# Performance work log

Hardware: AMD Instinct MI355X
Metric: run time of the kernel (lower is better)

The kernel has to match this reference:

```python
import jax, jax.numpy as jnp
import numpy as np

# Config mirrors init_kwargs
D_IN, D_OUT, HEADS, SEQ, BATCH = 1024, 64, 16, 2048, 2


def setup_inputs() -> dict:
    key = jax.random.key(0)
    kx, kq, kk, kv = jax.random.split(key, 4)
    scale = 1.0 / np.sqrt(D_IN)
    x = jax.random.normal(kx, (BATCH, SEQ, D_IN), dtype=jnp.float32)
    # Stacked per-head projection weights, [H, d_in, d_out] (qkv_bias=False)
    Wq = jax.random.normal(kq, (HEADS, D_IN, D_OUT), dtype=jnp.float32) * scale
    Wk = jax.random.normal(kk, (HEADS, D_IN, D_OUT), dtype=jnp.float32) * scale
    Wv = jax.random.normal(kv, (HEADS, D_IN, D_OUT), dtype=jnp.float32) * scale
    return {"x": x, "Wq": Wq, "Wk": Wk, "Wv": Wv}


def reference(x, Wq, Wk, Wv):
    # x: [B, S, d_in]; W*: [H, d_in, d_out]
    q = jnp.einsum("bsd,hde->bhse", x, Wq)
    k = jnp.einsum("bsd,hde->bhse", x, Wk)
    v = jnp.einsum("bsd,hde->bhse", x, Wv)
    scores = jnp.einsum("bhse,bhte->bhst", q, k) / jnp.sqrt(
        jnp.asarray(D_OUT, dtype=q.dtype)
    )
    S = x.shape[1]
    causal = jnp.tril(jnp.ones((S, S), dtype=bool))  # [S, S]
    scores = jnp.where(causal[None, None], scores, -jnp.inf)
    attn = jax.nn.softmax(scores, axis=-1)  # dropout=0.0 (eval)
    ctx = jnp.einsum("bhst,bhte->bhse", attn, v)  # [B, H, S, d_out]
    # concat heads on last dim -> [B, S, H*d_out]
    B, H, S2, E = ctx.shape
    return jnp.transpose(ctx, (0, 2, 1, 3)).reshape(B, S2, H * E)
```

## Files before the change

kernel.cpp:

```cpp
#include <hip/hip_runtime.h>
#include <hip/hip_bf16.h>
#include <math.h>

#define BATCH 2
#define SEQ   2048
#define DIN   1024
#define HEADS 16
#define EDIM  64

#define NX   (BATCH*SEQ*DIN)
#define NW   (3*HEADS*DIN*EDIM)
#define NQKV (BATCH*HEADS*SEQ*EDIM)

#define QSCALE 0.18033688011112042f

typedef __attribute__((ext_vector_type(8))) short short8;
typedef __attribute__((ext_vector_type(4))) float f32x4;

static __device__ __forceinline__ ushort f2bf(float f) {
    __hip_bfloat16 h = __float2bfloat16(f);
    return *reinterpret_cast<ushort*>(&h);
}

__global__ __launch_bounds__(256) void prep(
    const float* __restrict__ x, const float* __restrict__ Wq,
    const float* __restrict__ Wk, const float* __restrict__ Wv,
    ushort* __restrict__ xb, ushort* __restrict__ wt)
{
    const int t = threadIdx.x;
    if (blockIdx.x < 1024) {
        const int v0 = blockIdx.x * 256 + t;
#pragma unroll
        for (int i = 0; i < 4; ++i) {
            int i4 = (v0 + i * 262144) * 4;
            float4 f = *(const float4*)(x + i4);
            ushort4 o;
            o.x = f2bf(f.x); o.y = f2bf(f.y); o.z = f2bf(f.z); o.w = f2bf(f.w);
            *(ushort4*)(xb + i4) = o;
        }
    } else {
        const int bid = blockIdx.x - 1024;
        const int dt  = bid & 15;
        const int h   = (bid >> 4) & 15;
        const int mat = bid >> 8;

        const float* W = (mat == 0) ? Wq : (mat == 1) ? Wk : Wv;
        const float* src = W + ((size_t)h * DIN + dt * 64) * EDIM;
        ushort* dst = wt + ((size_t)(mat * HEADS + h) * EDIM) * DIN + dt * 64;

        __shared__ ushort T[64][68];
#pragma unroll
        for (int i = 0; i < 16; ++i) {
            int v = t + i * 256;
            int d = v >> 6, e = v & 63;
            T[d][e] = f2bf(src[(size_t)d * EDIM + e]);
        }
        __syncthreads();
#pragma unroll
        for (int i = 0; i < 4; ++i) {
            int v = t + i * 256;
            int e = v >> 4, d4 = (v & 15) << 2;
            ushort4 ov;
            ov.x = T[d4 + 0][e]; ov.y = T[d4 + 1][e];
            ov.z = T[d4 + 2][e]; ov.w = T[d4 + 3][e];
            *(ushort4*)&dst[(size_t)e * DIN + d4] = ov;
        }
    }
}

__global__ __launch_bounds__(256) void qkv_mfma(
    const ushort* __restrict__ xb, const ushort* __restrict__ wt,
    ushort* __restrict__ qkv)
{
    const int bid0 = blockIdx.x;
    const int swz  = (bid0 & 7) * 192 + (bid0 >> 3);
    const int h    = swz & 15;
    const int mt   = (swz >> 4) & 15;
    const int b    = (swz >> 8) & 1;
    const int mat  = swz >> 9;

    const ushort* xbase = xb + (size_t)(b * SEQ + mt * 128) * DIN;
    const ushort* wbase = wt + ((size_t)(mat * HEADS + h) * EDIM) * DIN;

    __shared__ ushort Xs[128][72];
    __shared__ ushort Ws[64][72];

    const int t    = threadIdx.x;
    const int lane = t & 63;
    const int wm0  = (t >> 6) * 32;
    const int fr   = lane & 15;
    const int fk   = (lane >> 4) * 8;

    ushort4 xr[8], wr[4];
#pragma unroll
    for (int i = 0; i < 8; ++i) { int v = t + i * 256; xr[i] = *(const ushort4*)&xbase[(size_t)(v >> 4) * DIN + ((v & 15) << 2)]; }
#pragma unroll
    for (int i = 0; i < 4; ++i) { int v = t + i * 256; wr[i] = *(const ushort4*)&wbase[(size_t)(v >> 4) * DIN + ((v & 15) << 2)]; }

    f32x4 acc[2][4];
#pragma unroll
    for (int i = 0; i < 2; ++i)
#pragma unroll
        for (int j = 0; j < 4; ++j) acc[i][j] = (f32x4)0.f;

    for (int kt = 0; kt < DIN / 64; ++kt) {
        __syncthreads();
#pragma unroll
        for (int i = 0; i < 8; ++i) { int v = t + i * 256; *(ushort4*)&Xs[v >> 4][(v & 15) << 2] = xr[i]; }
#pragma unroll
        for (int i = 0; i < 4; ++i) { int v = t + i * 256; *(ushort4*)&Ws[v >> 4][(v & 15) << 2] = wr[i]; }
        __syncthreads();
        if (kt + 1 < DIN / 64) {
            const int k0 = (kt + 1) * 64;
#pragma unroll
            for (int i = 0; i < 8; ++i) { int v = t + i * 256; xr[i] = *(const ushort4*)&xbase[(size_t)(v >> 4) * DIN + k0 + ((v & 15) << 2)]; }
#pragma unroll
            for (int i = 0; i < 4; ++i) { int v = t + i * 256; wr[i] = *(const ushort4*)&wbase[(size_t)(v >> 4) * DIN + k0 + ((v & 15) << 2)]; }
        }
        short8 a[2][2], bf[4][2];
#pragma unroll
        for (int rb = 0; rb < 2; ++rb)
#pragma unroll
            for (int kk = 0; kk < 2; ++kk)
                a[rb][kk] = *(const short8*)&Xs[wm0 + rb * 16 + fr][kk * 32 + fk];
#pragma unroll
        for (int cf = 0; cf < 4; ++cf)
#pragma unroll
            for (int kk = 0; kk < 2; ++kk)
                bf[cf][kk] = *(const short8*)&Ws[cf * 16 + fr][kk * 32 + fk];
#pragma unroll
        for (int kk = 0; kk < 2; ++kk)
#pragma unroll
            for (int rb = 0; rb < 2; ++rb)
#pragma unroll
                for (int cf = 0; cf < 4; ++cf)
                    acc[rb][cf] = __builtin_amdgcn_mfma_f32_16x16x32_bf16(a[rb][kk], bf[cf][kk], acc[rb][cf], 0, 0, 0);
    }

    const int rg = (lane >> 4) * 4;
    if (mat < 2) {
        const float sc = (mat == 0) ? QSCALE : 1.0f;
        ushort* dst = qkv + (size_t)mat * NQKV
                    + ((size_t)((b * HEADS + h) * SEQ) + mt * 128) * EDIM;
#pragma unroll
        for (int rb = 0; rb < 2; ++rb)
#pragma unroll
            for (int cf = 0; cf < 4; ++cf)
#pragma unroll
                for (int i = 0; i < 4; ++i)
                    dst[(size_t)(wm0 + rb * 16 + rg + i) * EDIM + cf * 16 + fr] = f2bf(acc[rb][cf][i] * sc);
    } else {
        ushort* vtb = qkv + (size_t)2 * NQKV + ((size_t)((b * HEADS + h) * EDIM)) * SEQ;
#pragma unroll
        for (int rb = 0; rb < 2; ++rb)
#pragma unroll
            for (int cf = 0; cf < 4; ++cf) {
                ushort4 ov;
                ov.x = f2bf(acc[rb][cf][0]); ov.y = f2bf(acc[rb][cf][1]);
                ov.z = f2bf(acc[rb][cf][2]); ov.w = f2bf(acc[rb][cf][3]);
                *(ushort4*)&vtb[(size_t)(cf * 16 + fr) * SEQ + mt * 128 + wm0 + rb * 16 + rg] = ov;
            }
    }
}

__global__ __launch_bounds__(512) void flash_mfma(
    const ushort* __restrict__ q, const ushort* __restrict__ k,
    const ushort* __restrict__ vt, float* __restrict__ out)
{
    const int bid = blockIdx.x;
    const int it  = 15 - (bid >> 5);
    const int bh  = bid & 31;
    const int b   = bh >> 4;
    const int h   = bh & 15;
    const int KT  = 2 * it + 2;

    const ushort* Qb  = q  + ((size_t)((b * HEADS + h) * SEQ) + it * 128) * EDIM;
    const ushort* Kb  = k  + ((size_t)((b * HEADS + h) * SEQ)) * EDIM;
    const ushort* Vtb = vt + ((size_t)((b * HEADS + h) * EDIM)) * SEQ;

    __shared__ ushort Ks_[2][64][72];
    __shared__ ushort Vs_[2][64][72];
    __shared__ ushort Ps_[8][16][72];

    const int t    = threadIdx.x;
    const int lane = t & 63;
    const int w    = t >> 6;
    const int fr   = lane & 15;
    const int fk   = (lane >> 4) * 8;
    const int rg   = (lane >> 4) * 4;

    const int srow = t >> 3;
    const int scol = (t & 7) * 8;

    const int wrow0 = it * 128 + w * 16;
    const int lastT = wrow0 >> 6;
    const int qrow  = wrow0 + fr;

    short8 qf[2];
#pragma unroll
    for (int kk = 0; kk < 2; ++kk)
        qf[kk] = *(const short8*)&Qb[(size_t)(w * 16 + fr) * EDIM + kk * 32 + fk];

    f32x4 o_[4];
#pragma unroll
    for (int cf = 0; cf < 4; ++cf) o_[cf] = (f32x4)0.f;
    float lpart = 0.f;

    uint4 krv = *(const uint4*)&Kb[(size_t)srow * EDIM + scol];
    uint4 vrv = *(const uint4*)&Vtb[(size_t)srow * SEQ + scol];
    *(uint4*)&Ks_[0][srow][scol] = krv;
    *(uint4*)&Vs_[0][srow][scol] = vrv;
    __syncthreads();

    for (int kt = 0; kt < KT; ++kt) {
        const int cur = kt & 1;

        if (kt + 1 < KT) {
            krv = *(const uint4*)&Kb[(size_t)((kt + 1) * 64 + srow) * EDIM + scol];
            vrv = *(const uint4*)&Vtb[(size_t)srow * SEQ + (kt + 1) * 64 + scol];
        }

        if (kt <= lastT) {
            f32x4 s[4];
#pragma unroll
            for (int cf = 0; cf < 4; ++cf) s[cf] = (f32x4)0.f;
#pragma unroll
            for (int cf = 0; cf < 4; ++cf)
#pragma unroll
                for (int kk = 0; kk < 2; ++kk) {
                    short8 kf = *(const short8*)&Ks_[cur][cf * 16 + fr][kk * 32 + fk];
                    s[cf] = __builtin_amdgcn_mfma_f32_16x16x32_bf16(kf, qf[kk], s[cf], 0, 0, 0);
                }

            const bool dm = (kt == lastT);
            if (dm) {
#pragma unroll
                for (int cf = 0; cf < 4; ++cf)
#pragma unroll
                    for (int i = 0; i < 4; ++i) {
                        int kpos = kt * 64 + cf * 16 + rg + i;
                        if (kpos > qrow) s[cf][i] = -1e30f;
                    }
            }

            float ls = 0.f;
#pragma unroll
            for (int cf = 0; cf < 4; ++cf) {
                float p0 = __builtin_amdgcn_exp2f(s[cf][0]);
                float p1 = __builtin_amdgcn_exp2f(s[cf][1]);
                float p2 = __builtin_amdgcn_exp2f(s[cf][2]);
                float p3 = __builtin_amdgcn_exp2f(s[cf][3]);
                ls += (p0 + p1) + (p2 + p3);
                uint2 pk;
                pk.x = (uint)f2bf(p0) | ((uint)f2bf(p1) << 16);
                pk.y = (uint)f2bf(p2) | ((uint)f2bf(p3) << 16);
                *(uint2*)&Ps_[w][fr][cf * 16 + rg] = pk;
            }
            lpart += ls;

            short8 pf[2];
#pragma unroll
            for (int kb = 0; kb < 2; ++kb)
                pf[kb] = *(const short8*)&Ps_[w][fr][kb * 32 + fk];
#pragma unroll
            for (int cf = 0; cf < 4; ++cf)
#pragma unroll
                for (int kb = 0; kb < 2; ++kb) {
                    short8 vf = *(const short8*)&Vs_[cur][cf * 16 + fr][kb * 32 + fk];
                    o_[cf] = __builtin_amdgcn_mfma_f32_16x16x32_bf16(vf, pf[kb], o_[cf], 0, 0, 0);
                }
        }

        if (kt + 1 < KT) {
            const int nxt = cur ^ 1;
            *(uint4*)&Ks_[nxt][srow][scol] = krv;
            *(uint4*)&Vs_[nxt][srow][scol] = vrv;
            __syncthreads();
        }
    }

    float ls = lpart;
    ls += __shfl_xor(ls, 16);
    ls += __shfl_xor(ls, 32);
    const float inv = 1.f / ls;

    float* rowp = out + ((size_t)(b * SEQ + qrow)) * (HEADS * EDIM) + h * EDIM;
#pragma unroll
    for (int cf = 0; cf < 4; ++cf) {
        f32x4 ov = o_[cf] * inv;
        *(f32x4*)&rowp[cf * 16 + rg] = ov;
    }
}

extern "C" void kernel_launch(void* const* d_in, const int* in_sizes, int n_in,
                              void* d_out, int out_size, void* d_ws, size_t ws_size,
                              hipStream_t stream) {
    const float* x  = (const float*)d_in[0];
    const float* Wq = (const float*)d_in[1];
    const float* Wk = (const float*)d_in[2];
    const float* Wv = (const float*)d_in[3];
    float* out = (float*)d_out;

    ushort* xb  = (ushort*)d_ws;
    ushort* wt  = xb + NX;
    ushort* qkv = wt + NW;

    prep<<<1792, 256, 0, stream>>>(x, Wq, Wk, Wv, xb, wt);
    qkv_mfma<<<3 * BATCH * HEADS * (SEQ / 128), 256, 0, stream>>>(xb, wt, qkv);
    flash_mfma<<<BATCH * HEADS * (SEQ / 128), 512, 0, stream>>>(
        qkv, qkv + NQKV, qkv + (size_t)2 * NQKV, out);
}
```

Baseline: 100.3 us.

## Retile QKV projection to 128x128 blocks with direct global-to-LDS loads

Replaces the per-head 128x64 QKV projection tiles with 128x128 output tiles spanning two heads, using a 2x2 warp layout with 64x64 per-warp accumulators. Operand loads now go straight from global memory into LDS via the global_load_lds builtin instead of staging through registers. The aim is more arithmetic per loaded byte and fewer register and VALU copy instructions. In exchange the register-level prefetch of the next K tile is gone, so loads are no longer overlapped with MFMA, and the unpadded LDS rows may cause bank conflicts.

```diff
diff --git a/kernel.cpp b/kernel.cpp
--- a/kernel.cpp
+++ b/kernel.cpp
@@ -20,6 +20,14 @@
 static __device__ __forceinline__ ushort f2bf(float f) {
     __hip_bfloat16 h = __float2bfloat16(f);
     return *reinterpret_cast<ushort*>(&h);
+}
+
+static __device__ __forceinline__ void gload16(const void* g, void* l) {
+    void* gv = const_cast<void*>(g);
+    __builtin_amdgcn_global_load_lds(
+        (__attribute__((address_space(1))) void*)gv,
+        (__attribute__((address_space(3))) void*)l,
+        16, 0, 0);
 }
 
 __global__ __launch_bounds__(256) void prep(
@@ -68,97 +76,92 @@
     }
 }
 
-__global__ __launch_bounds__(256) void qkv_mfma(
+__global__ __launch_bounds__(256) void qkv_gemm(
     const ushort* __restrict__ xb, const ushort* __restrict__ wt,
     ushort* __restrict__ qkv)
 {
     const int bid0 = blockIdx.x;
-    const int swz  = (bid0 & 7) * 192 + (bid0 >> 3);
-    const int h    = swz & 15;
-    const int mt   = (swz >> 4) & 15;
-    const int b    = (swz >> 8) & 1;
-    const int mat  = swz >> 9;
-
-    const ushort* xbase = xb + (size_t)(b * SEQ + mt * 128) * DIN;
-    const ushort* wbase = wt + ((size_t)(mat * HEADS + h) * EDIM) * DIN;
-
-    __shared__ ushort Xs[128][72];
-    __shared__ ushort Ws[64][72];
+    const int swz  = (bid0 & 7) * 96 + (bid0 >> 3);
+    const int nt   = swz % 24;
+    const int mt   = swz / 24;
+    const int m0 = mt * 128, n0 = nt * 128;
+    const int mat = nt >> 3;
+    const int b   = mt >> 4;
+
+    __shared__ ushort As[128][64];
+    __shared__ ushort Bs[128][64];
 
     const int t    = threadIdx.x;
     const int lane = t & 63;
-    const int wm0  = (t >> 6) * 32;
+    const int w    = t >> 6;
+    const int wr   = w >> 1, wc = w & 1;
     const int fr   = lane & 15;
     const int fk   = (lane >> 4) * 8;
-
-    ushort4 xr[8], wr[4];
-#pragma unroll
-    for (int i = 0; i < 8; ++i) { int v = t + i * 256; xr[i] = *(const ushort4*)&xbase[(size_t)(v >> 4) * DIN + ((v & 15) << 2)]; }
-#pragma unroll
-    for (int i = 0; i < 4; ++i) { int v = t + i * 256; wr[i] = *(const ushort4*)&wbase[(size_t)(v >> 4) * DIN + ((v & 15) << 2)]; }
-
-    f32x4 acc[2][4];
-#pragma unroll
-    for (int i = 0; i < 2; ++i)
+    const int rg   = (lane >> 4) * 4;
+
+    const ushort* xbase = xb + (size_t)m0 * DIN;
+    const ushort* wbase = wt + (size_t)n0 * DIN;
+
+    const int lrow = lane >> 3;
+    const int lcol = (lane & 7) * 8;
+
+    f32x4 acc[4][4];
+#pragma unroll
+    for (int i = 0; i < 4; ++i)
 #pragma unroll
         for (int j = 0; j < 4; ++j) acc[i][j] = (f32x4)0.f;
 
     for (int kt = 0; kt < DIN / 64; ++kt) {
+        const int k0 = kt * 64;
         __syncthreads();
 #pragma unroll
-        for (int i = 0; i < 8; ++i) { int v = t + i * 256; *(ushort4*)&Xs[v >> 4][(v & 15) << 2] = xr[i]; }
-#pragma unroll
-        for (int i = 0; i < 4; ++i) { int v = t + i * 256; *(ushort4*)&Ws[v >> 4][(v & 15) << 2] = wr[i]; }
+        for (int j = 0; j < 4; ++j) {
+            const int c = w * 4 + j;
+            gload16(&xbase[(size_t)(c * 8 + lrow) * DIN + k0 + lcol], &As[c * 8][0]);
+            gload16(&wbase[(size_t)(c * 8 + lrow) * DIN + k0 + lcol], &Bs[c * 8][0]);
+        }
         __syncthreads();
-        if (kt + 1 < DIN / 64) {
-            const int k0 = (kt + 1) * 64;
-#pragma unroll
-            for (int i = 0; i < 8; ++i) { int v = t + i * 256; xr[i] = *(const ushort4*)&xbase[(size_t)(v >> 4) * DIN + k0 + ((v & 15) << 2)]; }
-#pragma unroll
-            for (int i = 0; i < 4; ++i) { int v = t + i * 256; wr[i] = *(const ushort4*)&wbase[(size_t)(v >> 4) * DIN + k0 + ((v & 15) << 2)]; }
-        }
-        short8 a[2][2], bf[4][2];
-#pragma unroll
-        for (int rb = 0; rb < 2; ++rb)
-#pragma unroll
-            for (int kk = 0; kk < 2; ++kk)
-                a[rb][kk] = *(const short8*)&Xs[wm0 + rb * 16 + fr][kk * 32 + fk];
-#pragma unroll
-        for (int cf = 0; cf < 4; ++cf)
-#pragma unroll
-            for (int kk = 0; kk < 2; ++kk)
-                bf[cf][kk] = *(const short8*)&Ws[cf * 16 + fr][kk * 32 + fk];
+
+        short8 a[4][2], bfr[4][2];
+#pragma unroll
+        for (int rb = 0; rb < 4; ++rb)
+#pragma unroll
+            for (int kk = 0; kk < 2; ++kk) {
+                a[rb][kk]   = *(const short8*)&As[wr * 64 + rb * 16 + fr][kk * 32 + fk];
+                bfr[rb][kk] = *(const short8*)&Bs[wc * 64 + rb * 16 + fr][kk * 32 + fk];
+            }
 #pragma unroll
         for (int kk = 0; kk < 2; ++kk)
 #pragma unroll
-            for (int rb = 0; rb < 2; ++rb)
+            for (int rb = 0; rb < 4; ++rb)
 #pragma unroll
                 for (int cf = 0; cf < 4; ++cf)
-                    acc[rb][cf] = __builtin_amdgcn_mfma_f32_16x16x32_bf16(a[rb][kk], bf[cf][kk], acc[rb][cf], 0, 0, 0);
-    }
-
-    const int rg = (lane >> 4) * 4;
+                    acc[rb][cf] = __builtin_amdgcn_mfma_f32_16x16x32_bf16(a[rb][kk], bfr[cf][kk], acc[rb][cf], 0, 0, 0);
+    }
+
+    const int h  = (nt & 7) * 2 + wc;
+    const int s0 = (m0 & 2047) + wr * 64;
     if (mat < 2) {
         const float sc = (mat == 0) ? QSCALE : 1.0f;
         ushort* dst = qkv + (size_t)mat * NQKV
-                    + ((size_t)((b * HEADS + h) * SEQ) + mt * 128) * EDIM;
-#pragma unroll
-        for (int rb = 0; rb < 2; ++rb)
+                    + ((size_t)((b * HEADS + h) * SEQ) + s0) * EDIM;
+#pragma unroll
+        for (int rb = 0; rb < 4; ++rb)
 #pragma unroll
             for (int cf = 0; cf < 4; ++cf)
 #pragma unroll
                 for (int i = 0; i < 4; ++i)
-                    dst[(size_t)(wm0 + rb * 16 + rg + i) * EDIM + cf * 16 + fr] = f2bf(acc[rb][cf][i] * sc);
+                    dst[(size_t)(rb * 16 + rg + i) * EDIM + cf * 16 + fr] = f2bf(acc[rb][cf][i] * sc);
     } else {
-        ushort* vtb = qkv + (size_t)2 * NQKV + ((size_t)((b * HEADS + h) * EDIM)) * SEQ;
-#pragma unroll
-        for (int rb = 0; rb < 2; ++rb)
+        ushort* vtb = qkv + (size_t)2 * NQKV + ((size_t)(b * HEADS + h) * EDIM) * SEQ;
+#pragma unroll
+        for (int rb = 0; rb < 4; ++rb)
 #pragma unroll
             for (int cf = 0; cf < 4; ++cf) {
                 ushort4 ov;
                 ov.x = f2bf(acc[rb][cf][0]); ov.y = f2bf(acc[rb][cf][1]);
                 ov.z = f2bf(acc[rb][cf][2]); ov.w = f2bf(acc[rb][cf][3]);
-                *(ushort4*)&vtb[(size_t)(cf * 16 + fr) * SEQ + mt * 128 + wm0 + rb * 16 + rg] = ov;
+                *(ushort4*)&vtb[(size_t)(cf * 16 + fr) * SEQ + s0 + rb * 16 + rg] = ov;
             }
     }
 }
@@ -306,7 +309,7 @@
     ushort* qkv = wt + NW;
 
     prep<<<1792, 256, 0, stream>>>(x, Wq, Wk, Wv, xb, wt);
-    qkv_mfma<<<3 * BATCH * HEADS * (SEQ / 128), 256, 0, stream>>>(xb, wt, qkv);
+    qkv_gemm<<<768, 256, 0, stream>>>(xb, wt, qkv);
     flash_mfma<<<BATCH * HEADS * (SEQ / 128), 512, 0, stream>>>(
         qkv, qkv + NQKV, qkv + (size_t)2 * NQKV, out);
 }
```

After: 107.9 us. 1.08x slower.
